# Kernel tuning notes

Measured on AMD Instinct MI355X. Metric: run time of the kernel, lower is better.

The kernel has to match this reference:

```python
import jax, jax.numpy as jnp
from jax import lax
import numpy as np

B, C, H, W = 32, 256, 56, 56
G1, G2 = 64, 4          # groups for 3x3 convs, number of parallel convs / 1x1 groups
EPS = 1e-5
DN = ('NCHW', 'OIHW', 'NCHW')


def setup_inputs() -> dict:
    key = jax.random.key(0)
    it = iter(jax.random.split(key, 32))
    nk = lambda: next(it)
    n = lambda shape, s=0.05: jax.random.normal(nk(), shape, jnp.float32) * s
    u = lambda shape: jax.random.uniform(nk(), shape, jnp.float32, minval=0.5, maxval=1.5)
    inp = {'x': jax.random.normal(nk(), (B, C, H, W), jnp.float32)}
    inp.update(
        w1=n((G2, G1, C // G1, 3, 3), 0.1), b1=n((G2, G1)),
        bn1a_g=1.0 + n((C,)), bn1a_b=n((C,)), bn1a_m=n((C,)), bn1a_v=u((C,)),
        pw1=n((C, C // G2, 1, 1), 0.1), pb1=n((C,)),
        bn1b_g=1.0 + n((C,)), bn1b_b=n((C,)), bn1b_m=n((C,)), bn1b_v=u((C,)),
        w2=n((G2, G1, C // G1, 3, 3), 0.1), b2=n((G2, G1)),
        bn2a_g=1.0 + n((C,)), bn2a_b=n((C,)), bn2a_m=n((C,)), bn2a_v=u((C,)),
        pw2=n((C, C // G2, 1, 1), 0.1), pb2=n((C,)),
        bn2b_g=1.0 + n((C,)), bn2b_b=n((C,)), bn2b_m=n((C,)), bn2b_v=u((C,)),
    )
    return inp


def _bn_relu(x, g, b, m, v):
    # inference-mode BatchNorm2d + ReLU, fused into one affine + relu
    inv = g / jnp.sqrt(v + EPS)
    return jax.nn.relu(x * inv[None, :, None, None] + (b - m * inv)[None, :, None, None])


def _gconv3x3(x, w, b):
    # Faithful to: [Conv2d(Cin, g1, k=3, p=1, groups=g1) for _ in range(g2)] then concat(dim=1).
    # Implemented as ONE grouped conv (feature_group_count=g1) followed by a cheap channel permute
    # to recover torch's concat ordering (conv-index major, group minor).
    g2, g1, cpg = w.shape[0], w.shape[1], w.shape[2]
    # combined weight: out channel k*g2 + i (group-major) uses conv i, group k
    Wc = jnp.transpose(w, (1, 0, 2, 3, 4)).reshape(g1 * g2, cpg, 3, 3)
    y = lax.conv_general_dilated(x, Wc, (1, 1), ((1, 1), (1, 1)),
                                 feature_group_count=g1, dimension_numbers=DN)
    Bx, _, Hy, Wy = y.shape
    # (g, i) ordering -> torch concat (i, g) ordering
    y = y.reshape(Bx, g1, g2, Hy, Wy).transpose(0, 2, 1, 3, 4).reshape(Bx, g1 * g2, Hy, Wy)
    return y + b.reshape(g1 * g2)[None, :, None, None]


def _pwconv(x, w, b):
    # Conv2d(C, C, k=1, groups=G2)
    y = lax.conv_general_dilated(x, w, (1, 1), 'VALID',
                                 feature_group_count=G2, dimension_numbers=DN)
    return y + b[None, :, None, None]


def reference(x, w1, b1, bn1a_g, bn1a_b, bn1a_m, bn1a_v, pw1, pb1,
              bn1b_g, bn1b_b, bn1b_m, bn1b_v,
              w2, b2, bn2a_g, bn2a_b, bn2a_m, bn2a_v, pw2, pb2,
              bn2b_g, bn2b_b, bn2b_m, bn2b_v):
    h = _gconv3x3(x, w1, b1)
    h = _bn_relu(h, bn1a_g, bn1a_b, bn1a_m, bn1a_v)
    h = _pwconv(h, pw1, pb1)
    h = _bn_relu(h, bn1b_g, bn1b_b, bn1b_m, bn1b_v)
    h = _gconv3x3(h, w2, b2)
    h = _bn_relu(h, bn2a_g, bn2a_b, bn2a_m, bn2a_v)
    h = _pwconv(h, pw2, pb2)
    h = _bn_relu(h, bn2b_g, bn2b_b, bn2b_m, bn2b_v)
    return h
```

## Files before the change

### kernel.cpp

```cpp
#include <hip/hip_runtime.h>

#define HW 3136
#define SHS 232

__global__ __launch_bounds__(256, 2) void fused_stage(
    const float* __restrict__ in,
    const float* __restrict__ gw,
    const float* __restrict__ gb,
    const float* __restrict__ bnag, const float* __restrict__ bnab,
    const float* __restrict__ bnam, const float* __restrict__ bnav,
    const float* __restrict__ pw,
    const float* __restrict__ pb,
    const float* __restrict__ bnbg, const float* __restrict__ bnbb,
    const float* __restrict__ bnbm, const float* __restrict__ bnbv,
    float* __restrict__ out)
{
    __shared__ float sH[64 * SHS];
    __shared__ float sW[64 * 64];

    const int tid = threadIdx.x;
    const int blk = blockIdx.x;
    const int t   = blk % 14;
    const int g   = (blk / 14) & 3;
    const int b   = blk / 56;
    const int y0  = t * 4;

    {
        const int o  = tid & 63;
        const int c0 = (tid >> 6) * 16;
        const float* src = pw + (size_t)(g * 64 + o) * 64 + c0;
        float4 v0 = *(const float4*)(src + 0);
        float4 v1 = *(const float4*)(src + 4);
        float4 v2 = *(const float4*)(src + 8);
        float4 v3 = *(const float4*)(src + 12);
        float tmp[16] = {v0.x, v0.y, v0.z, v0.w, v1.x, v1.y, v1.z, v1.w,
                         v2.x, v2.y, v2.z, v2.w, v3.x, v3.y, v3.z, v3.w};
#pragma unroll
        for (int j = 0; j < 16; ++j)
            sW[(c0 + j) * 64 + o] = tmp[j];
    }

    const int k  = tid >> 2;
    const int xs = tid & 3;
    const int x0 = xs * 14;

    float wr[36];
    {
        const float4* w4 = (const float4*)(gw + (size_t)(g * 64 + k) * 36);
#pragma unroll
        for (int j = 0; j < 9; ++j) {
            float4 v = w4[j];
            wr[4*j+0] = v.x; wr[4*j+1] = v.y; wr[4*j+2] = v.z; wr[4*j+3] = v.w;
        }
    }

    float acc[4][14];
#pragma unroll
    for (int r = 0; r < 4; ++r)
#pragma unroll
        for (int xx = 0; xx < 14; ++xx) acc[r][xx] = 0.f;

#pragma unroll
    for (int cc = 0; cc < 4; ++cc) {
        const float* chp = in + ((size_t)(b * 256 + k * 4 + cc)) * HW;
#pragma unroll
        for (int ry = 0; ry < 6; ++ry) {
            const int gy = y0 - 1 + ry;
            if ((unsigned)gy >= 56u) continue;
            const float* rp = chp + gy * 56;
            float rr[16];
            rr[0]  = (x0 > 0)       ? rp[x0 - 1]  : 0.f;
            rr[15] = (x0 + 14 < 56) ? rp[x0 + 14] : 0.f;
#pragma unroll
            for (int j = 0; j < 7; ++j) {
                float2 v = *(const float2*)(rp + x0 + 2 * j);
                rr[1 + 2*j] = v.x; rr[2 + 2*j] = v.y;
            }
            const int rlo = (ry >= 2) ? ry - 2 : 0;
            const int rhi = (ry <= 3) ? ry : 3;
#pragma unroll
            for (int r = 0; r < 4; ++r) {
                if (r < rlo || r > rhi) continue;
                const int dy = ry - r;
                const float w0 = wr[cc*9 + dy*3 + 0];
                const float w1 = wr[cc*9 + dy*3 + 1];
                const float w2 = wr[cc*9 + dy*3 + 2];
#pragma unroll
                for (int xx = 0; xx < 14; ++xx)
                    acc[r][xx] = fmaf(w2, rr[xx+2],
                                 fmaf(w1, rr[xx+1],
                                 fmaf(w0, rr[xx], acc[r][xx])));
            }
        }
    }

    {
        const int c = g * 64 + k;
        const float sc = bnag[c] * rsqrtf(bnav[c] + 1e-5f);
        const float sh = fmaf(gb[c], sc, bnab[c] - bnam[c] * sc);
#pragma unroll
        for (int r = 0; r < 4; ++r)
#pragma unroll
            for (int j = 0; j < 7; ++j) {
                float v0 = fmaxf(fmaf(acc[r][2*j],   sc, sh), 0.f);
                float v1 = fmaxf(fmaf(acc[r][2*j+1], sc, sh), 0.f);
                *(float2*)&sH[k * SHS + r * 56 + x0 + 2*j] = make_float2(v0, v1);
            }
    }
    __syncthreads();

    const int og = tid >> 4;
    const int pg = tid & 15;
    const int p0 = pg * 14;

    float a2[4][14];
#pragma unroll
    for (int i = 0; i < 4; ++i)
#pragma unroll
        for (int xx = 0; xx < 14; ++xx) a2[i][xx] = 0.f;

    for (int c = 0; c < 64; ++c) {
        const float4 wv = *(const float4*)&sW[c * 64 + og * 4];
        float hr[14];
#pragma unroll
        for (int j = 0; j < 7; ++j) {
            float2 v = *(const float2*)&sH[c * SHS + p0 + 2*j];
            hr[2*j] = v.x; hr[2*j+1] = v.y;
        }
#pragma unroll
        for (int xx = 0; xx < 14; ++xx) {
            a2[0][xx] = fmaf(wv.x, hr[xx], a2[0][xx]);
            a2[1][xx] = fmaf(wv.y, hr[xx], a2[1][xx]);
            a2[2][xx] = fmaf(wv.z, hr[xx], a2[2][xx]);
            a2[3][xx] = fmaf(wv.w, hr[xx], a2[3][xx]);
        }
    }

#pragma unroll
    for (int i = 0; i < 4; ++i) {
        const int o = g * 64 + og * 4 + i;
        const float sc = bnbg[o] * rsqrtf(bnbv[o] + 1e-5f);
        const float sh = fmaf(pb[o], sc, bnbb[o] - bnbm[o] * sc);
        float* op = out + ((size_t)(b * 256 + o)) * HW + y0 * 56 + p0;
#pragma unroll
        for (int j = 0; j < 7; ++j) {
            float v0 = fmaxf(fmaf(a2[i][2*j],   sc, sh), 0.f);
            float v1 = fmaxf(fmaf(a2[i][2*j+1], sc, sh), 0.f);
            *(float2*)(op + 2*j) = make_float2(v0, v1);
        }
    }
}

extern "C" void kernel_launch(void* const* d_in, const int* in_sizes, int n_in,
                              void* d_out, int out_size, void* d_ws, size_t ws_size,
                              hipStream_t stream) {
    const float* x     = (const float*)d_in[0];
    const float* w1    = (const float*)d_in[1];
    const float* b1    = (const float*)d_in[2];
    const float* bn1ag = (const float*)d_in[3];
    const float* bn1ab = (const float*)d_in[4];
    const float* bn1am = (const float*)d_in[5];
    const float* bn1av = (const float*)d_in[6];
    const float* pw1   = (const float*)d_in[7];
    const float* pb1   = (const float*)d_in[8];
    const float* bn1bg = (const float*)d_in[9];
    const float* bn1bb = (const float*)d_in[10];
    const float* bn1bm = (const float*)d_in[11];
    const float* bn1bv = (const float*)d_in[12];
    const float* w2    = (const float*)d_in[13];
    const float* b2    = (const float*)d_in[14];
    const float* bn2ag = (const float*)d_in[15];
    const float* bn2ab = (const float*)d_in[16];
    const float* bn2am = (const float*)d_in[17];
    const float* bn2av = (const float*)d_in[18];
    const float* pw2   = (const float*)d_in[19];
    const float* pb2   = (const float*)d_in[20];
    const float* bn2bg = (const float*)d_in[21];
    const float* bn2bb = (const float*)d_in[22];
    const float* bn2bm = (const float*)d_in[23];
    const float* bn2bv = (const float*)d_in[24];

    float* mid  = (float*)d_ws;
    float* outp = (float*)d_out;

    const int grid = 32 * 4 * 14;

    fused_stage<<<grid, 256, 0, stream>>>(x,   w1, b1, bn1ag, bn1ab, bn1am, bn1av,
                                          pw1, pb1, bn1bg, bn1bb, bn1bm, bn1bv, mid);
    fused_stage<<<grid, 256, 0, stream>>>(mid, w2, b2, bn2ag, bn2ab, bn2am, bn2av,
                                          pw2, pb2, bn2bg, bn2bb, bn2bm, bn2bv, outp);
}
```

Before: 477.1 us.

## Halve row tile to two rows, raise occupancy, and group-major block ordering

Each block now covers 2 output rows instead of 4, which doubles the grid and halves the shared-memory intermediate tile and per-thread accumulators, so launch bounds can request 3 blocks per SM. The block index is remapped so the 4 channel groups of neighbouring spatial tiles run close together, which should improve L2 reuse of the input rows. Input rows are loaded into registers before the FMAs so loads can overlap. The cost is a larger halo overhead: 4 input rows are read per 2 output rows instead of 6 per 4, and the pointwise stage gets less reuse per shared-memory load.

```diff
diff --git a/kernel.cpp b/kernel.cpp
--- a/kernel.cpp
+++ b/kernel.cpp
@@ -1,9 +1,9 @@
 #include <hip/hip_runtime.h>
 
 #define HW 3136
-#define SHS 232
-
-__global__ __launch_bounds__(256, 2) void fused_stage(
+#define SHS 116
+
+__global__ __launch_bounds__(256, 3) void fused_stage(
     const float* __restrict__ in,
     const float* __restrict__ gw,
     const float* __restrict__ gb,
@@ -15,15 +15,18 @@
     const float* __restrict__ bnbm, const float* __restrict__ bnbv,
     float* __restrict__ out)
 {
-    __shared__ float sH[64 * SHS];
-    __shared__ float sW[64 * 64];
+    __shared__ __align__(16) float sH[64 * SHS];
+    __shared__ __align__(16) float sW[64 * 64];
 
     const int tid = threadIdx.x;
     const int blk = blockIdx.x;
-    const int t   = blk % 14;
-    const int g   = (blk / 14) & 3;
-    const int b   = blk / 56;
-    const int y0  = t * 4;
+    const int x8 = blk & 7;
+    const int r8 = blk >> 3;
+    const int g  = r8 & 3;
+    const int s  = (r8 >> 2) * 8 + x8;
+    const int t  = s % 28;
+    const int b  = s / 28;
+    const int y0 = t * 2;
 
     {
         const int o  = tid & 63;
@@ -54,42 +57,49 @@
         }
     }
 
-    float acc[4][14];
-#pragma unroll
-    for (int r = 0; r < 4; ++r)
+    float acc[2][14];
+#pragma unroll
+    for (int r = 0; r < 2; ++r)
 #pragma unroll
         for (int xx = 0; xx < 14; ++xx) acc[r][xx] = 0.f;
 
 #pragma unroll
     for (int cc = 0; cc < 4; ++cc) {
         const float* chp = in + ((size_t)(b * 256 + k * 4 + cc)) * HW;
-#pragma unroll
-        for (int ry = 0; ry < 6; ++ry) {
+        float rw[4][16];
+#pragma unroll
+        for (int ry = 0; ry < 4; ++ry) {
             const int gy = y0 - 1 + ry;
-            if ((unsigned)gy >= 56u) continue;
-            const float* rp = chp + gy * 56;
-            float rr[16];
-            rr[0]  = (x0 > 0)       ? rp[x0 - 1]  : 0.f;
-            rr[15] = (x0 + 14 < 56) ? rp[x0 + 14] : 0.f;
-#pragma unroll
-            for (int j = 0; j < 7; ++j) {
-                float2 v = *(const float2*)(rp + x0 + 2 * j);
-                rr[1 + 2*j] = v.x; rr[2 + 2*j] = v.y;
+            if ((unsigned)gy < 56u) {
+                const float* rp = chp + gy * 56;
+                rw[ry][0]  = (x0 > 0)       ? rp[x0 - 1]  : 0.f;
+                rw[ry][15] = (x0 + 14 < 56) ? rp[x0 + 14] : 0.f;
+#pragma unroll
+                for (int j = 0; j < 7; ++j) {
+                    float2 v = *(const float2*)(rp + x0 + 2 * j);
+                    rw[ry][1 + 2*j] = v.x; rw[ry][2 + 2*j] = v.y;
+                }
+            } else {
+#pragma unroll
+                for (int j = 0; j < 16; ++j) rw[ry][j] = 0.f;
             }
+        }
+#pragma unroll
+        for (int ry = 0; ry < 4; ++ry) {
             const int rlo = (ry >= 2) ? ry - 2 : 0;
-            const int rhi = (ry <= 3) ? ry : 3;
-#pragma unroll
-            for (int r = 0; r < 4; ++r) {
-                if (r < rlo || r > rhi) continue;
-                const int dy = ry - r;
+            const int rhi = (ry <= 1) ? ry : 1;
+#pragma unroll
+            for (int rr = 0; rr < 2; ++rr) {
+                if (rr < rlo || rr > rhi) continue;
+                const int dy = ry - rr;
                 const float w0 = wr[cc*9 + dy*3 + 0];
                 const float w1 = wr[cc*9 + dy*3 + 1];
                 const float w2 = wr[cc*9 + dy*3 + 2];
 #pragma unroll
                 for (int xx = 0; xx < 14; ++xx)
-                    acc[r][xx] = fmaf(w2, rr[xx+2],
-                                 fmaf(w1, rr[xx+1],
-                                 fmaf(w0, rr[xx], acc[r][xx])));
+                    acc[rr][xx] = fmaf(w2, rw[ry][xx+2],
+                                  fmaf(w1, rw[ry][xx+1],
+                                  fmaf(w0, rw[ry][xx], acc[rr][xx])));
             }
         }
     }
@@ -99,7 +109,7 @@
         const float sc = bnag[c] * rsqrtf(bnav[c] + 1e-5f);
         const float sh = fmaf(gb[c], sc, bnab[c] - bnam[c] * sc);
 #pragma unroll
-        for (int r = 0; r < 4; ++r)
+        for (int r = 0; r < 2; ++r)
 #pragma unroll
             for (int j = 0; j < 7; ++j) {
                 float v0 = fmaxf(fmaf(acc[r][2*j],   sc, sh), 0.f);
@@ -109,18 +119,19 @@
     }
     __syncthreads();
 
-    const int og = tid >> 4;
-    const int pg = tid & 15;
+    const int og = tid >> 3;
+    const int pg = tid & 7;
     const int p0 = pg * 14;
 
-    float a2[4][14];
-#pragma unroll
-    for (int i = 0; i < 4; ++i)
+    float a2[2][14];
+#pragma unroll
+    for (int i = 0; i < 2; ++i)
 #pragma unroll
         for (int xx = 0; xx < 14; ++xx) a2[i][xx] = 0.f;
 
+#pragma unroll 2
     for (int c = 0; c < 64; ++c) {
-        const float4 wv = *(const float4*)&sW[c * 64 + og * 4];
+        const float2 wv = *(const float2*)&sW[c * 64 + og * 2];
         float hr[14];
 #pragma unroll
         for (int j = 0; j < 7; ++j) {
@@ -131,14 +142,12 @@
         for (int xx = 0; xx < 14; ++xx) {
             a2[0][xx] = fmaf(wv.x, hr[xx], a2[0][xx]);
             a2[1][xx] = fmaf(wv.y, hr[xx], a2[1][xx]);
-            a2[2][xx] = fmaf(wv.z, hr[xx], a2[2][xx]);
-            a2[3][xx] = fmaf(wv.w, hr[xx], a2[3][xx]);
-        }
-    }
-
-#pragma unroll
-    for (int i = 0; i < 4; ++i) {
-        const int o = g * 64 + og * 4 + i;
+        }
+    }
+
+#pragma unroll
+    for (int i = 0; i < 2; ++i) {
+        const int o = g * 64 + og * 2 + i;
         const float sc = bnbg[o] * rsqrtf(bnbv[o] + 1e-5f);
         const float sh = fmaf(pb[o], sc, bnbb[o] - bnbm[o] * sc);
         float* op = out + ((size_t)(b * 256 + o)) * HW + y0 * 56 + p0;
@@ -183,7 +192,7 @@
     float* mid  = (float*)d_ws;
     float* outp = (float*)d_out;
 
-    const int grid = 32 * 4 * 14;
+    const int grid = 32 * 4 * 28;
 
     fused_stage<<<grid, 256, 0, stream>>>(x,   w1, b1, bn1ag, bn1ab, bn1am, bn1av,
                                           pw1, pb1, bn1bg, bn1bb, bn1bm, bn1bv, mid);
```

Measured after the change: 824.8 us. +72.9%, slower.
